# Optimization experiments

Hardware: AMD Instinct MI355X
Metric: run time of the kernel (lower is better)

## Reference

```python
import jax, jax.numpy as jnp
from jax import lax
import numpy as np

B, ENC, H, DE, T = 16384, 512, 256, 32, 64


def setup_inputs() -> dict:
    key = jax.random.key(0)
    ks = jax.random.split(key, 12)
    s = lambda fan: 1.0 / np.sqrt(fan)
    return {
        "encoded_input_series": jax.random.normal(ks[0], (B, ENC), jnp.float32),
        "final_x_val": jax.random.normal(ks[1], (B, 1), jnp.float32),
        # embed_func: Dense(DE) applied to scalar input (last dim = 1)
        "W_emb": jax.random.normal(ks[2], (1, DE), jnp.float32) * s(1),
        "b_emb": jnp.zeros((DE,), jnp.float32),
        # encode_reshape layer: Dense(H) on encoded series -> initial h
        "W_enc": jax.random.normal(ks[3], (ENC, H), jnp.float32) * s(ENC),
        "b_enc": jnp.zeros((H,), jnp.float32),
        # LSTM cell params (Keras gate order i, f, c, o)
        "W_k": jax.random.normal(ks[4], (DE, 4 * H), jnp.float32) * s(DE),
        "W_r": jax.random.normal(ks[5], (H, 4 * H), jnp.float32) * s(H),
        "b_lstm": jnp.concatenate([jnp.zeros((H,)), jnp.ones((H,)), jnp.zeros((2 * H,))]).astype(jnp.float32),
        # reduce layer: Dense(1)
        "W_red": jax.random.normal(ks[6], (H, 1), jnp.float32) * s(H),
        "b_red": jnp.zeros((1,), jnp.float32),
        "decode_length": T,
    }


def reference(encoded_input_series, final_x_val, W_emb, b_emb, W_enc, b_enc,
              W_k, W_r, b_lstm, W_red, b_red, decode_length):
    Hdim = W_r.shape[0]
    # initial hidden state from encoder summary; cell state zero-initialized
    h0 = encoded_input_series @ W_enc + b_enc            # [B, H]
    c0 = jnp.zeros_like(h0)
    # initial decoder input: embed of last observed value
    x0 = final_x_val @ W_emb + b_emb                     # [B, DE]

    def step(carry, _):
        h, c, x = carry
        gates = x @ W_k + h @ W_r + b_lstm               # [B, 4H]
        i, f, cb, o = jnp.split(gates, 4, axis=-1)
        c_new = jax.nn.sigmoid(f) * c + jax.nn.sigmoid(i) * jnp.tanh(cb)
        h_new = jax.nn.sigmoid(o) * jnp.tanh(c_new)
        y = h_new @ W_red + b_red                        # [B, 1]
        x_next = y @ W_emb + b_emb
        return (h_new, c_new, x_next), y[:, 0]

    _, ys = lax.scan(step, (h0, c0, x0), None, length=decode_length)
    return ys.T                                          # [B, T]
```

## Files before the change

kernel.cpp:

```cpp
#include <hip/hip_runtime.h>
#include <hip/hip_bf16.h>
#include <math.h>


typedef _Float16 f16x8 __attribute__((ext_vector_type(8)));
typedef float f32x4 __attribute__((ext_vector_type(4)));

#define DEV __device__ __forceinline__

constexpr int ENC = 512;
constexpr int HD  = 256;
constexpr int DE  = 32;
constexpr int TT  = 64;
constexpr int NG  = 4 * HD;
constexpr int NKT = 8;
constexpr int TS  = 528;
constexpr int BR  = 32;
constexpr int NMT = 2;
constexpr int BPS = 12;
constexpr int WRS = 36;

constexpr float L2E = 1.44269504088896f;

DEV bool is_f32(const void* blstm) {
  return ((const unsigned*)blstm)[256] == 0x3F800000u;
}
DEV float ldf(const void* p, size_t i, bool f32) {
  return f32 ? ((const float*)p)[i]
             : __bfloat162float(((const __hip_bfloat16*)p)[i]);
}
DEV float gscale(int n) {
  return ((n >> 8) == 2) ? (2.0f * L2E) : L2E;
}
DEV void split2h(float v, _Float16& hi, _Float16& lo) {
  hi = (_Float16)v;
  lo = (_Float16)(v - (float)hi);
}
DEV void ld8cvt2h(const void* p, size_t i, bool f32, f16x8& hi, f16x8& lo) {
  if (f32) {
    const f32x4* q = (const f32x4*)((const float*)p + i);
    f32x4 u0 = q[0], u1 = q[1];
#pragma unroll
    for (int j = 0; j < 4; ++j) {
      float a = u0[j], b = u1[j];
      _Float16 ah = (_Float16)a, bh = (_Float16)b;
      hi[j] = ah; hi[4 + j] = bh;
      lo[j] = (_Float16)(a - (float)ah); lo[4 + j] = (_Float16)(b - (float)bh);
    }
  } else {
    const __hip_bfloat16* s = (const __hip_bfloat16*)p + i;
#pragma unroll
    for (int j = 0; j < 8; ++j) {
      float a = __bfloat162float(s[j]);
      _Float16 ah = (_Float16)a;
      hi[j] = ah;
      lo[j] = (_Float16)(a - (float)ah);
    }
  }
}
DEV f16x8 load8h(const _Float16* p) {
  return *reinterpret_cast<const f16x8*>(p);
}

__global__ __launch_bounds__(256) void pack_vec(const void* __restrict__ wemb,
                                                const void* __restrict__ bemb,
                                                const void* __restrict__ wk,
                                                const void* __restrict__ bl,
                                                const void* __restrict__ bredp,
                                                float* __restrict__ wk2n,
                                                float* __restrict__ wk2s,
                                                float* __restrict__ bps,
                                                float* __restrict__ bp2P) {
  const bool f32 = is_f32(bl);
  int n = blockIdx.x * 256 + threadIdx.x;
  if (n >= NG) return;
  float s1 = 0.f, s2 = 0.f;
  for (int j = 0; j < DE; ++j) {
    float wkv = ldf(wk, (size_t)j * NG + n, f32);
    s1 += ldf(wemb, j, f32) * wkv;
    s2 += ldf(bemb, j, f32) * wkv;
  }
  float b = s2 + ldf(bl, n, f32);
  float sc = gscale(n);
  wk2n[n] = s1;
  wk2s[n] = s1 * sc;
  bps[n]  = b * sc;
  int g = n >> 8, rem = n & 255;
  int hh = (rem >> 4) & 1;
  int cbase = (rem & 0xE0) | (rem & 15);
  int nf = g * 2 + hh;
  bp2P[cbase * BPS + nf] = (b + ldf(bredp, 0, f32) * s1) * sc;
}

__global__ __launch_bounds__(256) void pack_w(const void* __restrict__ wr,
                                              const void* __restrict__ bl,
                                              const void* __restrict__ wred,
                                              const float* __restrict__ wk2n,
                                              _Float16* __restrict__ d0,
                                              _Float16* __restrict__ d1) {
  const bool f32 = is_f32(bl);
  int idx = blockIdx.x * 256 + threadIdx.x;
  if (idx >= NKT * 64 * 64) return;
  int lane = idx & 63, tile = idx >> 6;
  int nt = tile & 63, ks = tile >> 6;
  int kb = ks * 32 + ((lane >> 4) << 3);
  int n  = (nt << 4) + (lane & 15);
  float wn = wk2n[n];
  float sc = gscale(n);
#pragma unroll
  for (int j = 0; j < 8; ++j) {
    int k = kb + j;
    float v = ldf(wr, (size_t)k * NG + n, f32);
    d0[idx * 8 + j] = (_Float16)(v * sc);
    d1[idx * 8 + j] = (_Float16)((v + ldf(wred, k, f32) * wn) * sc);
  }
}

__global__ __launch_bounds__(256) void pack_e(const void* __restrict__ we,
                                              const void* __restrict__ bl,
                                              _Float16* __restrict__ dhi,
                                              _Float16* __restrict__ dlo) {
  const bool f32 = is_f32(bl);
  int idx = blockIdx.x * 256 + threadIdx.x;
  if (idx >= 16 * 16 * 64) return;
  int lane = idx & 63, tile = idx >> 6;
  int nt = tile & 15, ks = tile >> 4;
  int kb = ks * 32 + ((lane >> 4) << 3);
  int n  = (nt << 4) + (lane & 15);
#pragma unroll
  for (int j = 0; j < 8; ++j) {
    float v = ldf(we, (size_t)(kb + j) * HD + n, f32);
    _Float16 h, l;
    split2h(v, h, l);
    dhi[idx * 8 + j] = h;
    dlo[idx * 8 + j] = l;
  }
}

__global__ __launch_bounds__(512)
__attribute__((amdgpu_waves_per_eu(4, 4)))
void lstm_main(
    const void* __restrict__ enc,
    const void* __restrict__ fx,
    const void* __restrict__ benc,
    const void* __restrict__ blstm,
    const void* __restrict__ wred,
    const void* __restrict__ bredp,
    const _Float16* __restrict__ pW0,
    const _Float16* __restrict__ pW1,
    const _Float16* __restrict__ pEhi,
    const _Float16* __restrict__ pElo,
    const float* __restrict__ wk2s,
    const float* __restrict__ bps,
    const float* __restrict__ bp2P,
    const int* __restrict__ dlen,
    void* __restrict__ out) {
  __shared__ __align__(16) _Float16 frag[2][NMT * NKT * TS];
  __shared__ __align__(16) float bp0L[NG];
  __shared__ __align__(16) float wk2L[NG];
  __shared__ __align__(16) float bp2P_l[HD * BPS];
  __shared__ __align__(16) float wredfP[16 * WRS];
  __shared__ __align__(16) float fxL[BR];

  const bool f32 = is_f32(blstm);
  const int tid  = threadIdx.x;
  const int w    = tid >> 6;
  const int lane = tid & 63;
  const int q    = lane >> 4;
  const int cl   = lane & 15;
  const int r0   = blockIdx.x * BR;
  int Tn = dlen[0];
  if (Tn < 1 || Tn > TT) Tn = TT;

  const int aoff = lane * 8;
  const int hwb = w * TS + q * 32 + 128 * (cl >> 3) + (cl & 7);
  const int cbase = w * 32 + cl;

  const int yrow  = tid >> 4, ypart = tid & 15;
  const int ybase = ((yrow >> 4) * NKT + (ypart >> 1)) * TS +
                    ((yrow & 15) + 16 * ((ypart & 1) * 2)) * 8;
  const int yws   = ypart * WRS;

  if (tid < HD) wredfP[(tid >> 4) * WRS + (tid & 15)] = ldf(wred, tid, f32);
  if (tid < BR) fxL[tid] = ldf(fx, r0 + tid, f32);
  bp0L[tid]        = bps[tid];
  bp0L[tid + 512]  = bps[tid + 512];
  wk2L[tid]        = wk2s[tid];
  wk2L[tid + 512]  = wk2s[tid + 512];
#pragma unroll
  for (int k = 0; k < HD * BPS / 512; ++k)
    bp2P_l[tid + k * 512] = bp2P[tid + k * 512];
  const float bredf = ldf(bredp, 0, f32);

  f32x4 acc0[NMT][2];
  {
    float be0 = ldf(benc, w * 32 + cl, f32);
    float be1 = ldf(benc, w * 32 + 16 + cl, f32);
#pragma unroll
    for (int mt = 0; mt < NMT; ++mt) {
      acc0[mt][0] = (f32x4){be0, be0, be0, be0};
      acc0[mt][1] = (f32x4){be1, be1, be1, be1};
    }
  }
  const size_t ebase = ((size_t)(w * 2) * 64 + lane) * 8;
#pragma unroll 1
  for (int ks = 0; ks < ENC / 32; ++ks) {
    f16x8 bh[2], bl2[2];
#pragma unroll
    for (int hh = 0; hh < 2; ++hh) {
      size_t fo = ebase + (size_t)(ks * 16 + hh) * 512;
      bh[hh]  = load8h(pEhi + fo);
      bl2[hh] = load8h(pElo + fo);
    }
#pragma unroll
    for (int mt = 0; mt < NMT; ++mt) {
      f16x8 ah, al;
      ld8cvt2h(enc, (size_t)(r0 + mt * 16 + cl) * ENC + ks * 32 + q * 8, f32, ah, al);
#pragma unroll
      for (int hh = 0; hh < 2; ++hh) {
        acc0[mt][hh] = __builtin_amdgcn_mfma_f32_16x16x32_f16(ah, bh[hh],  acc0[mt][hh], 0, 0, 0);
        acc0[mt][hh] = __builtin_amdgcn_mfma_f32_16x16x32_f16(al, bh[hh],  acc0[mt][hh], 0, 0, 0);
        acc0[mt][hh] = __builtin_amdgcn_mfma_f32_16x16x32_f16(ah, bl2[hh], acc0[mt][hh], 0, 0, 0);
      }
    }
  }
#pragma unroll
  for (int mt = 0; mt < NMT; ++mt)
#pragma unroll
    for (int hh = 0; hh < 2; ++hh)
#pragma unroll
      for (int r = 0; r < 4; ++r) {
        int idx = mt * NKT * TS + hwb + r * 8 + hh * 256;
        frag[0][idx] = (_Float16)acc0[mt][hh][r];
      }

  f32x4 cst[NMT][2];
#pragma unroll
  for (int mt = 0; mt < NMT; ++mt)
#pragma unroll
    for (int hh = 0; hh < 2; ++hh) cst[mt][hh] = (f32x4){0.f, 0.f, 0.f, 0.f};

  __syncthreads();

  const _Float16* wbase0 = pW0 + ((size_t)(w * 2) * 64 + lane) * 8;
  const _Float16* wbase1 = pW1 + ((size_t)(w * 2) * 64 + lane) * 8;

  int rb = 0;
#pragma unroll 1
  for (int t = 0; t < Tn; ++t) {
    const _Float16* FH = &frag[rb][0];
    _Float16* WH = &frag[rb ^ 1][0];

    f32x4 acc[NMT][8];
    if (t == 0) {
      f32x4 fxv[NMT];
#pragma unroll
      for (int mt = 0; mt < NMT; ++mt)
        fxv[mt] = *(const f32x4*)&fxL[mt * 16 + q * 4];
#pragma unroll
      for (int nf = 0; nf < 8; ++nf) {
        int col = (nf >> 1) * 256 + (nf & 1) * 16 + cbase;
        float bb = bp0L[col], wv = wk2L[col];
#pragma unroll
        for (int mt = 0; mt < NMT; ++mt) {
          f32x4 a;
#pragma unroll
          for (int r = 0; r < 4; ++r) a[r] = bb + fxv[mt][r] * wv;
          acc[mt][nf] = a;
        }
      }
    } else {
      f32x4 bA = *(const f32x4*)&bp2P_l[cbase * BPS];
      f32x4 bB = *(const f32x4*)&bp2P_l[cbase * BPS + 4];
#pragma unroll
      for (int nf = 0; nf < 8; ++nf) {
        float bb = (nf < 4) ? bA[nf & 3] : bB[nf & 3];
#pragma unroll
        for (int mt = 0; mt < NMT; ++mt) acc[mt][nf] = (f32x4){bb, bb, bb, bb};
      }
    }

    const _Float16* wb = (t == 0) ? wbase0 : wbase1;
#pragma unroll 1
    for (int j = 0; j < 8; ++j) {
      int ks = (j + w) & 7;
#pragma unroll
      for (int half = 0; half < 2; ++half) {
        f16x8 bc[4];
#pragma unroll
        for (int p = 0; p < 4; ++p)
          bc[p] = load8h(wb +
                         (size_t)(ks * 64 + (half * 2 + (p >> 1)) * 16 + (p & 1)) * 512);
#pragma unroll
        for (int mt = 0; mt < NMT; ++mt) {
          f16x8 ah = load8h(&FH[(mt * NKT + ks) * TS + aoff]);
          __builtin_amdgcn_s_setprio(1);
#pragma unroll
          for (int p = 0; p < 4; ++p)
            acc[mt][half * 4 + p] =
                __builtin_amdgcn_mfma_f32_16x16x32_f16(ah, bc[p], acc[mt][half * 4 + p], 0, 0, 0);
          __builtin_amdgcn_s_setprio(0);
        }
      }
    }

    if (t > 0) {
      float sum = 0.f;
#pragma unroll
      for (int jj = 0; jj < 2; ++jj) {
        f16x8 hv = load8h(&FH[ybase + jj * 128]);
        f32x4 wv0 = *(const f32x4*)&wredfP[yws + jj * 8];
        f32x4 wv1 = *(const f32x4*)&wredfP[yws + jj * 8 + 4];
#pragma unroll
        for (int j = 0; j < 4; ++j) {
          sum += (float)hv[j] * wv0[j];
          sum += (float)hv[4 + j] * wv1[j];
        }
      }
      sum += __shfl_xor(sum, 1);
      sum += __shfl_xor(sum, 2);
      sum += __shfl_xor(sum, 4);
      sum += __shfl_xor(sum, 8);
      if (ypart == 0) {
        float y = sum + bredf;
        size_t oi = (size_t)(r0 + yrow) * TT + (t - 1);
        if (f32) ((float*)out)[oi] = y;
        else     ((__hip_bfloat16*)out)[oi] = __float2bfloat16(y);
      }
    }

#pragma unroll
    for (int mt = 0; mt < NMT; ++mt)
#pragma unroll
      for (int hh = 0; hh < 2; ++hh)
#pragma unroll
        for (int r = 0; r < 4; ++r) {
          float gi = acc[mt][0 + hh][r];
          float gf = acc[mt][2 + hh][r];
          float gc = acc[mt][4 + hh][r];
          float go = acc[mt][6 + hh][r];
          float P = __builtin_amdgcn_exp2f(-gi);
          float F = __builtin_amdgcn_exp2f(-gf);
          float Q = __builtin_amdgcn_exp2f(-gc);
          float S = __builtin_amdgcn_exp2f(-go);
          float p1 = 1.0f + P, q1 = 1.0f + Q, f1 = 1.0f + F, s1 = 1.0f + S;
          float pq = p1 * q1;
          float num = cst[mt][hh][r] * pq + (1.0f - Q) * f1;
          float cn  = num * __builtin_amdgcn_rcpf(f1 * pq);
          cst[mt][hh][r] = cn;
          float R = __builtin_amdgcn_exp2f(-2.0f * L2E * cn);
          float hn = (1.0f - R) * __builtin_amdgcn_rcpf(s1 * (1.0f + R));
          int idx = mt * NKT * TS + hwb + r * 8 + hh * 256;
          WH[idx] = (_Float16)hn;
        }
    __syncthreads();
    rb ^= 1;
  }

  {
    const _Float16* FH = &frag[rb][0];
    float sum = 0.f;
#pragma unroll
    for (int jj = 0; jj < 2; ++jj) {
      f16x8 hv = load8h(&FH[ybase + jj * 128]);
      f32x4 wv0 = *(const f32x4*)&wredfP[yws + jj * 8];
      f32x4 wv1 = *(const f32x4*)&wredfP[yws + jj * 8 + 4];
#pragma unroll
      for (int j = 0; j < 4; ++j) {
        sum += (float)hv[j] * wv0[j];
        sum += (float)hv[4 + j] * wv1[j];
      }
    }
    sum += __shfl_xor(sum, 1);
    sum += __shfl_xor(sum, 2);
    sum += __shfl_xor(sum, 4);
    sum += __shfl_xor(sum, 8);
    if (ypart == 0) {
      float y = sum + bredf;
      size_t oi = (size_t)(r0 + yrow) * TT + (Tn - 1);
      if (f32) ((float*)out)[oi] = y;
      else     ((__hip_bfloat16*)out)[oi] = __float2bfloat16(y);
    }
  }
}

extern "C" void kernel_launch(void* const* d_in, const int* in_sizes, int n_in,
                              void* d_out, int out_size, void* d_ws, size_t ws_size,
                              hipStream_t stream) {
  const void* enc  = d_in[0];
  const void* fx   = d_in[1];
  const void* wemb = d_in[2];
  const void* bemb = d_in[3];
  const void* wenc = d_in[4];
  const void* benc = d_in[5];
  const void* wk   = d_in[6];
  const void* wr   = d_in[7];
  const void* bl   = d_in[8];
  const void* wred = d_in[9];
  const void* bred = d_in[10];
  const int* dlen  = (const int*)d_in[11];

  _Float16* pW0 = (_Float16*)d_ws;
  _Float16* pW1 = pW0 + NKT * 64 * 64 * 8;
  _Float16* pEhi = pW1 + NKT * 64 * 64 * 8;
  _Float16* pElo = pEhi + 16 * 16 * 64 * 8;
  float* wk2n = (float*)(pElo + 16 * 16 * 64 * 8);
  float* wk2s = wk2n + NG;
  float* bps  = wk2s + NG;
  float* bp2P = bps + NG;

  pack_vec<<<4, 256, 0, stream>>>(wemb, bemb, wk, bl, bred, wk2n, wk2s, bps, bp2P);
  pack_w<<<128, 256, 0, stream>>>(wr, bl, wred, wk2n, pW0, pW1);
  pack_e<<<64, 256, 0, stream>>>(wenc, bl, pEhi, pElo);

  int nblocks = in_sizes[1] / BR;
  lstm_main<<<nblocks, 512, 0, stream>>>(enc, fx, benc, bl, wred, bred,
                                         pW0, pW1, pEhi, pElo, wk2s, bps, bp2P,
                                         dlen, d_out);
}
```

Before: 877.6 us.

## Switch LSTM kernel from 16x16x32 to 32x32x16 MFMA tiles

Replaces the 16x16x32 f16 MFMA tiling with 32x32x16 MFMA for both the encoder projection and the recurrent gate matmul. Each wave now owns one 32-column hidden slice across all four gates, so the gate nonlinearity reads i/f/c/o directly from four accumulators. Weight packing, the shared-memory fragment layout and the bias/wk vectors are repacked to match. The aim is fewer MFMA issues and fewer LDS A-fragment loads per step, at the cost of a different register footprint and LDS access pattern.

```diff
diff --git a/kernel.cpp b/kernel.cpp
--- a/kernel.cpp
+++ b/kernel.cpp
@@ -5,6 +5,7 @@
 
 typedef _Float16 f16x8 __attribute__((ext_vector_type(8)));
 typedef float f32x4 __attribute__((ext_vector_type(4)));
+typedef float f32x16 __attribute__((ext_vector_type(16)));
 
 #define DEV __device__ __forceinline__
 
@@ -13,11 +14,9 @@
 constexpr int DE  = 32;
 constexpr int TT  = 64;
 constexpr int NG  = 4 * HD;
-constexpr int NKT = 8;
-constexpr int TS  = 528;
+constexpr int NKS = 16;
+constexpr int TSZ = 520;
 constexpr int BR  = 32;
-constexpr int NMT = 2;
-constexpr int BPS = 12;
 constexpr int WRS = 36;
 
 constexpr float L2E = 1.44269504088896f;
@@ -68,8 +67,8 @@
                                                 const void* __restrict__ bl,
                                                 const void* __restrict__ bredp,
                                                 float* __restrict__ wk2n,
-                                                float* __restrict__ wk2s,
-                                                float* __restrict__ bps,
+                                                float* __restrict__ wk2P,
+                                                float* __restrict__ bp0P,
                                                 float* __restrict__ bp2P) {
   const bool f32 = is_f32(bl);
   int n = blockIdx.x * 256 + threadIdx.x;
@@ -82,14 +81,11 @@
   }
   float b = s2 + ldf(bl, n, f32);
   float sc = gscale(n);
+  int g = n >> 8, hcol = n & 255;
   wk2n[n] = s1;
-  wk2s[n] = s1 * sc;
-  bps[n]  = b * sc;
-  int g = n >> 8, rem = n & 255;
-  int hh = (rem >> 4) & 1;
-  int cbase = (rem & 0xE0) | (rem & 15);
-  int nf = g * 2 + hh;
-  bp2P[cbase * BPS + nf] = (b + ldf(bredp, 0, f32) * s1) * sc;
+  wk2P[hcol * 4 + g] = s1 * sc;
+  bp0P[hcol * 4 + g] = b * sc;
+  bp2P[hcol * 4 + g] = (b + ldf(bredp, 0, f32) * s1) * sc;
 }
 
 __global__ __launch_bounds__(256) void pack_w(const void* __restrict__ wr,
@@ -100,11 +96,11 @@
                                               _Float16* __restrict__ d1) {
   const bool f32 = is_f32(bl);
   int idx = blockIdx.x * 256 + threadIdx.x;
-  if (idx >= NKT * 64 * 64) return;
+  if (idx >= 512 * 64) return;
   int lane = idx & 63, tile = idx >> 6;
-  int nt = tile & 63, ks = tile >> 6;
-  int kb = ks * 32 + ((lane >> 4) << 3);
-  int n  = (nt << 4) + (lane & 15);
+  int nt = tile & 31, ks = tile >> 5;
+  int kb = ks * 16 + ((lane >> 5) << 3);
+  int n  = nt * 32 + (lane & 31);
   float wn = wk2n[n];
   float sc = gscale(n);
 #pragma unroll
@@ -122,11 +118,11 @@
                                               _Float16* __restrict__ dlo) {
   const bool f32 = is_f32(bl);
   int idx = blockIdx.x * 256 + threadIdx.x;
-  if (idx >= 16 * 16 * 64) return;
+  if (idx >= 256 * 64) return;
   int lane = idx & 63, tile = idx >> 6;
-  int nt = tile & 15, ks = tile >> 4;
-  int kb = ks * 32 + ((lane >> 4) << 3);
-  int n  = (nt << 4) + (lane & 15);
+  int nt = tile & 7, ks = tile >> 3;
+  int kb = ks * 16 + ((lane >> 5) << 3);
+  int n  = nt * 32 + (lane & 31);
 #pragma unroll
   for (int j = 0; j < 8; ++j) {
     float v = ldf(we, (size_t)(kb + j) * HD + n, f32);
@@ -150,15 +146,15 @@
     const _Float16* __restrict__ pW1,
     const _Float16* __restrict__ pEhi,
     const _Float16* __restrict__ pElo,
-    const float* __restrict__ wk2s,
-    const float* __restrict__ bps,
+    const float* __restrict__ wk2P,
+    const float* __restrict__ bp0P,
     const float* __restrict__ bp2P,
     const int* __restrict__ dlen,
     void* __restrict__ out) {
-  __shared__ __align__(16) _Float16 frag[2][NMT * NKT * TS];
-  __shared__ __align__(16) float bp0L[NG];
-  __shared__ __align__(16) float wk2L[NG];
-  __shared__ __align__(16) float bp2P_l[HD * BPS];
+  __shared__ __align__(16) _Float16 frag[2][NKS * TSZ];
+  __shared__ __align__(16) float bp0L[HD * 4];
+  __shared__ __align__(16) float wk2L[HD * 4];
+  __shared__ __align__(16) float bp2L[HD * 4];
   __shared__ __align__(16) float wredfP[16 * WRS];
   __shared__ __align__(16) float fxL[BR];
 
@@ -166,84 +162,59 @@
   const int tid  = threadIdx.x;
   const int w    = tid >> 6;
   const int lane = tid & 63;
-  const int q    = lane >> 4;
-  const int cl   = lane & 15;
+  const int cl32 = lane & 31;
+  const int l5   = lane >> 5;
   const int r0   = blockIdx.x * BR;
   int Tn = dlen[0];
   if (Tn < 1 || Tn > TT) Tn = TT;
 
   const int aoff = lane * 8;
-  const int hwb = w * TS + q * 32 + 128 * (cl >> 3) + (cl & 7);
-  const int cbase = w * 32 + cl;
+  const int hcol = w * 32 + cl32;
+  const int hwb = (2 * w + (cl32 >> 4)) * TSZ + 256 * ((cl32 >> 3) & 1) +
+                  (cl32 & 7);
 
   const int yrow  = tid >> 4, ypart = tid & 15;
-  const int ybase = ((yrow >> 4) * NKT + (ypart >> 1)) * TS +
-                    ((yrow & 15) + 16 * ((ypart & 1) * 2)) * 8;
+  const int ybase = ypart * TSZ + yrow * 8;
   const int yws   = ypart * WRS;
 
   if (tid < HD) wredfP[(tid >> 4) * WRS + (tid & 15)] = ldf(wred, tid, f32);
   if (tid < BR) fxL[tid] = ldf(fx, r0 + tid, f32);
-  bp0L[tid]        = bps[tid];
-  bp0L[tid + 512]  = bps[tid + 512];
-  wk2L[tid]        = wk2s[tid];
-  wk2L[tid + 512]  = wk2s[tid + 512];
-#pragma unroll
-  for (int k = 0; k < HD * BPS / 512; ++k)
-    bp2P_l[tid + k * 512] = bp2P[tid + k * 512];
+  bp0L[tid]        = bp0P[tid];
+  bp0L[tid + 512]  = bp0P[tid + 512];
+  bp2L[tid]        = bp2P[tid];
+  bp2L[tid + 512]  = bp2P[tid + 512];
+  wk2L[tid]        = wk2P[tid];
+  wk2L[tid + 512]  = wk2P[tid + 512];
   const float bredf = ldf(bredp, 0, f32);
 
-  f32x4 acc0[NMT][2];
+  f32x16 acc0;
   {
-    float be0 = ldf(benc, w * 32 + cl, f32);
-    float be1 = ldf(benc, w * 32 + 16 + cl, f32);
-#pragma unroll
-    for (int mt = 0; mt < NMT; ++mt) {
-      acc0[mt][0] = (f32x4){be0, be0, be0, be0};
-      acc0[mt][1] = (f32x4){be1, be1, be1, be1};
-    }
-  }
-  const size_t ebase = ((size_t)(w * 2) * 64 + lane) * 8;
+    float be = ldf(benc, hcol, f32);
+#pragma unroll
+    for (int r = 0; r < 16; ++r) acc0[r] = be;
+  }
 #pragma unroll 1
-  for (int ks = 0; ks < ENC / 32; ++ks) {
-    f16x8 bh[2], bl2[2];
-#pragma unroll
-    for (int hh = 0; hh < 2; ++hh) {
-      size_t fo = ebase + (size_t)(ks * 16 + hh) * 512;
-      bh[hh]  = load8h(pEhi + fo);
-      bl2[hh] = load8h(pElo + fo);
-    }
-#pragma unroll
-    for (int mt = 0; mt < NMT; ++mt) {
-      f16x8 ah, al;
-      ld8cvt2h(enc, (size_t)(r0 + mt * 16 + cl) * ENC + ks * 32 + q * 8, f32, ah, al);
-#pragma unroll
-      for (int hh = 0; hh < 2; ++hh) {
-        acc0[mt][hh] = __builtin_amdgcn_mfma_f32_16x16x32_f16(ah, bh[hh],  acc0[mt][hh], 0, 0, 0);
-        acc0[mt][hh] = __builtin_amdgcn_mfma_f32_16x16x32_f16(al, bh[hh],  acc0[mt][hh], 0, 0, 0);
-        acc0[mt][hh] = __builtin_amdgcn_mfma_f32_16x16x32_f16(ah, bl2[hh], acc0[mt][hh], 0, 0, 0);
-      }
-    }
-  }
-#pragma unroll
-  for (int mt = 0; mt < NMT; ++mt)
-#pragma unroll
-    for (int hh = 0; hh < 2; ++hh)
-#pragma unroll
-      for (int r = 0; r < 4; ++r) {
-        int idx = mt * NKT * TS + hwb + r * 8 + hh * 256;
-        frag[0][idx] = (_Float16)acc0[mt][hh][r];
-      }
-
-  f32x4 cst[NMT][2];
-#pragma unroll
-  for (int mt = 0; mt < NMT; ++mt)
-#pragma unroll
-    for (int hh = 0; hh < 2; ++hh) cst[mt][hh] = (f32x4){0.f, 0.f, 0.f, 0.f};
+  for (int ks = 0; ks < ENC / 16; ++ks) {
+    size_t fo = ((size_t)(ks * 8 + w) * 64 + lane) * 8;
+    f16x8 bh  = load8h(pEhi + fo);
+    f16x8 bl2 = load8h(pElo + fo);
+    f16x8 ah, al;
+    ld8cvt2h(enc, (size_t)(r0 + cl32) * ENC + ks * 16 + l5 * 8, f32, ah, al);
+    acc0 = __builtin_amdgcn_mfma_f32_32x32x16_f16(ah, bh,  acc0, 0, 0, 0);
+    acc0 = __builtin_amdgcn_mfma_f32_32x32x16_f16(al, bh,  acc0, 0, 0, 0);
+    acc0 = __builtin_amdgcn_mfma_f32_32x32x16_f16(ah, bl2, acc0, 0, 0, 0);
+  }
+#pragma unroll
+  for (int reg = 0; reg < 16; ++reg) {
+    int row = (reg & 3) + 8 * (reg >> 2) + 4 * l5;
+    frag[0][hwb + row * 8] = (_Float16)acc0[reg];
+  }
+
+  float cst[16];
+#pragma unroll
+  for (int reg = 0; reg < 16; ++reg) cst[reg] = 0.f;
 
   __syncthreads();
-
-  const _Float16* wbase0 = pW0 + ((size_t)(w * 2) * 64 + lane) * 8;
-  const _Float16* wbase1 = pW1 + ((size_t)(w * 2) * 64 + lane) * 8;
 
   int rb = 0;
 #pragma unroll 1
@@ -251,64 +222,46 @@
     const _Float16* FH = &frag[rb][0];
     _Float16* WH = &frag[rb ^ 1][0];
 
-    f32x4 acc[NMT][8];
+    f32x16 acc[4];
     if (t == 0) {
-      f32x4 fxv[NMT];
-#pragma unroll
-      for (int mt = 0; mt < NMT; ++mt)
-        fxv[mt] = *(const f32x4*)&fxL[mt * 16 + q * 4];
-#pragma unroll
-      for (int nf = 0; nf < 8; ++nf) {
-        int col = (nf >> 1) * 256 + (nf & 1) * 16 + cbase;
-        float bb = bp0L[col], wv = wk2L[col];
-#pragma unroll
-        for (int mt = 0; mt < NMT; ++mt) {
-          f32x4 a;
-#pragma unroll
-          for (int r = 0; r < 4; ++r) a[r] = bb + fxv[mt][r] * wv;
-          acc[mt][nf] = a;
-        }
+      f32x4 b0 = *(const f32x4*)&bp0L[hcol * 4];
+      f32x4 wk = *(const f32x4*)&wk2L[hcol * 4];
+#pragma unroll
+      for (int reg = 0; reg < 16; ++reg) {
+        int row = (reg & 3) + 8 * (reg >> 2) + 4 * l5;
+        float fxr = fxL[row];
+#pragma unroll
+        for (int g = 0; g < 4; ++g) acc[g][reg] = b0[g] + fxr * wk[g];
       }
     } else {
-      f32x4 bA = *(const f32x4*)&bp2P_l[cbase * BPS];
-      f32x4 bB = *(const f32x4*)&bp2P_l[cbase * BPS + 4];
-#pragma unroll
-      for (int nf = 0; nf < 8; ++nf) {
-        float bb = (nf < 4) ? bA[nf & 3] : bB[nf & 3];
-#pragma unroll
-        for (int mt = 0; mt < NMT; ++mt) acc[mt][nf] = (f32x4){bb, bb, bb, bb};
-      }
-    }
-
-    const _Float16* wb = (t == 0) ? wbase0 : wbase1;
+      f32x4 bb = *(const f32x4*)&bp2L[hcol * 4];
+#pragma unroll
+      for (int g = 0; g < 4; ++g)
+#pragma unroll
+        for (int reg = 0; reg < 16; ++reg) acc[g][reg] = bb[g];
+    }
+
+    const _Float16* wb = (t == 0) ? pW0 : pW1;
 #pragma unroll 1
-    for (int j = 0; j < 8; ++j) {
-      int ks = (j + w) & 7;
-#pragma unroll
-      for (int half = 0; half < 2; ++half) {
-        f16x8 bc[4];
-#pragma unroll
-        for (int p = 0; p < 4; ++p)
-          bc[p] = load8h(wb +
-                         (size_t)(ks * 64 + (half * 2 + (p >> 1)) * 16 + (p & 1)) * 512);
-#pragma unroll
-        for (int mt = 0; mt < NMT; ++mt) {
-          f16x8 ah = load8h(&FH[(mt * NKT + ks) * TS + aoff]);
-          __builtin_amdgcn_s_setprio(1);
-#pragma unroll
-          for (int p = 0; p < 4; ++p)
-            acc[mt][half * 4 + p] =
-                __builtin_amdgcn_mfma_f32_16x16x32_f16(ah, bc[p], acc[mt][half * 4 + p], 0, 0, 0);
-          __builtin_amdgcn_s_setprio(0);
-        }
-      }
+    for (int j = 0; j < NKS; ++j) {
+      int ks = (j + 2 * w) & 15;
+      f16x8 ah = load8h(&FH[ks * TSZ + aoff]);
+      f16x8 bc[4];
+#pragma unroll
+      for (int g = 0; g < 4; ++g)
+        bc[g] = load8h(wb + ((size_t)(ks * 32 + g * 8 + w) * 64 + lane) * 8);
+      __builtin_amdgcn_s_setprio(1);
+#pragma unroll
+      for (int g = 0; g < 4; ++g)
+        acc[g] = __builtin_amdgcn_mfma_f32_32x32x16_f16(ah, bc[g], acc[g], 0, 0, 0);
+      __builtin_amdgcn_s_setprio(0);
     }
 
     if (t > 0) {
       float sum = 0.f;
 #pragma unroll
       for (int jj = 0; jj < 2; ++jj) {
-        f16x8 hv = load8h(&FH[ybase + jj * 128]);
+        f16x8 hv = load8h(&FH[ybase + jj * 256]);
         f32x4 wv0 = *(const f32x4*)&wredfP[yws + jj * 8];
         f32x4 wv1 = *(const f32x4*)&wredfP[yws + jj * 8 + 4];
 #pragma unroll
@@ -330,29 +283,25 @@
     }
 
 #pragma unroll
-    for (int mt = 0; mt < NMT; ++mt)
-#pragma unroll
-      for (int hh = 0; hh < 2; ++hh)
-#pragma unroll
-        for (int r = 0; r < 4; ++r) {
-          float gi = acc[mt][0 + hh][r];
-          float gf = acc[mt][2 + hh][r];
-          float gc = acc[mt][4 + hh][r];
-          float go = acc[mt][6 + hh][r];
-          float P = __builtin_amdgcn_exp2f(-gi);
-          float F = __builtin_amdgcn_exp2f(-gf);
-          float Q = __builtin_amdgcn_exp2f(-gc);
-          float S = __builtin_amdgcn_exp2f(-go);
-          float p1 = 1.0f + P, q1 = 1.0f + Q, f1 = 1.0f + F, s1 = 1.0f + S;
-          float pq = p1 * q1;
-          float num = cst[mt][hh][r] * pq + (1.0f - Q) * f1;
-          float cn  = num * __builtin_amdgcn_rcpf(f1 * pq);
-          cst[mt][hh][r] = cn;
-          float R = __builtin_amdgcn_exp2f(-2.0f * L2E * cn);
-          float hn = (1.0f - R) * __builtin_amdgcn_rcpf(s1 * (1.0f + R));
-          int idx = mt * NKT * TS + hwb + r * 8 + hh * 256;
-          WH[idx] = (_Float16)hn;
-        }
+    for (int reg = 0; reg < 16; ++reg) {
+      float gi = acc[0][reg];
+      float gf = acc[1][reg];
+      float gc = acc[2][reg];
+      float go = acc[3][reg];
+      float P = __builtin_amdgcn_exp2f(-gi);
+      float F = __builtin_amdgcn_exp2f(-gf);
+      float Q = __builtin_amdgcn_exp2f(-gc);
+      float S = __builtin_amdgcn_exp2f(-go);
+      float p1 = 1.0f + P, q1 = 1.0f + Q, f1 = 1.0f + F, s1 = 1.0f + S;
+      float pq = p1 * q1;
+      float num = cst[reg] * pq + (1.0f - Q) * f1;
+      float cn  = num * __builtin_amdgcn_rcpf(f1 * pq);
+      cst[reg] = cn;
+      float R = __builtin_amdgcn_exp2f(-2.0f * L2E * cn);
+      float hn = (1.0f - R) * __builtin_amdgcn_rcpf(s1 * (1.0f + R));
+      int row = (reg & 3) + 8 * (reg >> 2) + 4 * l5;
+      WH[hwb + row * 8] = (_Float16)hn;
+    }
     __syncthreads();
     rb ^= 1;
   }
@@ -362,7 +311,7 @@
     float sum = 0.f;
 #pragma unroll
     for (int jj = 0; jj < 2; ++jj) {
-      f16x8 hv = load8h(&FH[ybase + jj * 128]);
+      f16x8 hv = load8h(&FH[ybase + jj * 256]);
       f32x4 wv0 = *(const f32x4*)&wredfP[yws + jj * 8];
       f32x4 wv1 = *(const f32x4*)&wredfP[yws + jj * 8 + 4];
 #pragma unroll
@@ -401,20 +350,20 @@
   const int* dlen  = (const int*)d_in[11];
 
   _Float16* pW0 = (_Float16*)d_ws;
-  _Float16* pW1 = pW0 + NKT * 64 * 64 * 8;
-  _Float16* pEhi = pW1 + NKT * 64 * 64 * 8;
-  _Float16* pElo = pEhi + 16 * 16 * 64 * 8;
-  float* wk2n = (float*)(pElo + 16 * 16 * 64 * 8);
-  float* wk2s = wk2n + NG;
-  float* bps  = wk2s + NG;
-  float* bp2P = bps + NG;
-
-  pack_vec<<<4, 256, 0, stream>>>(wemb, bemb, wk, bl, bred, wk2n, wk2s, bps, bp2P);
+  _Float16* pW1 = pW0 + 512 * 64 * 8;
+  _Float16* pEhi = pW1 + 512 * 64 * 8;
+  _Float16* pElo = pEhi + 256 * 64 * 8;
+  float* wk2n = (float*)(pElo + 256 * 64 * 8);
+  float* wk2P = wk2n + NG;
+  float* bp0P = wk2P + NG;
+  float* bp2P = bp0P + NG;
+
+  pack_vec<<<4, 256, 0, stream>>>(wemb, bemb, wk, bl, bred, wk2n, wk2P, bp0P, bp2P);
   pack_w<<<128, 256, 0, stream>>>(wr, bl, wred, wk2n, pW0, pW1);
   pack_e<<<64, 256, 0, stream>>>(wenc, bl, pEhi, pElo);
 
   int nblocks = in_sizes[1] / BR;
   lstm_main<<<nblocks, 512, 0, stream>>>(enc, fx, benc, bl, wred, bred,
-                                         pW0, pW1, pEhi, pElo, wk2s, bps, bp2P,
+                                         pW0, pW1, pEhi, pElo, wk2P, bp0P, bp2P,
                                          dlen, d_out);
 }
```

Measured after the change: 917.1 us. 4.5% more time.
